# Performance work log

Measured on AMD Instinct MI355X. Metric: run time of the kernel, lower is better.

Reference implementation:

```python
import jax, jax.numpy as jnp
import numpy as np

N, P, IN_DIM, OUT_DIM = 8192, 16, 256, 128
HID = [512, 1024, 1024, 512]
MIN_VAR = 0.01


def setup_inputs() -> dict:
    key = jax.random.key(0)
    ks = jax.random.split(key, 12)
    s = 0.05
    inp = {
        "x": jax.random.normal(ks[0], (N, P, IN_DIM), dtype=jnp.float32),
        "mask": jnp.zeros((N, P), dtype=bool),
        # per-film input FiLM linears, stacked: [P, hid0, in_dim]
        "W_in": jax.random.normal(ks[1], (P, HID[0], IN_DIM), dtype=jnp.float32) * s,
        "b_in": jax.random.normal(ks[2], (P, HID[0]), dtype=jnp.float32) * s,
        # shared trunk layers hidden_dims[i] -> hidden_dims[i+1]
        "W1": jax.random.normal(ks[3], (HID[1], HID[0]), dtype=jnp.float32) * s,
        "b1": jax.random.normal(ks[4], (HID[1],), dtype=jnp.float32) * s,
        "W2": jax.random.normal(ks[5], (HID[2], HID[1]), dtype=jnp.float32) * s,
        "b2": jax.random.normal(ks[6], (HID[2],), dtype=jnp.float32) * s,
        "W3": jax.random.normal(ks[7], (HID[3], HID[2]), dtype=jnp.float32) * s,
        "b3": jax.random.normal(ks[8], (HID[3],), dtype=jnp.float32) * s,
        # per-film output FiLM linears: [P, 2*out_dim, hid_last]
        "W_out": jax.random.normal(ks[9], (P, 2 * OUT_DIM, HID[3]), dtype=jnp.float32) * s,
        "b_out": jax.random.normal(ks[10], (P, 2 * OUT_DIM), dtype=jnp.float32) * s,
    }
    return inp


def reference(x, mask, W_in, b_in, W1, b1, W2, b2, W3, b3, W_out, b_out):
    # per-film input linear (no activation after it, matching original)
    h = jnp.einsum("npd,phd->nph", x, W_in) + b_in            # [N,P,hid0]
    # shared trunk: activation after each layer
    h = jax.nn.relu(jnp.einsum("nph,oh->npo", h, W1) + b1)    # [N,P,hid1]
    h = jax.nn.relu(jnp.einsum("nph,oh->npo", h, W2) + b2)    # [N,P,hid2]
    h = jax.nn.relu(jnp.einsum("nph,oh->npo", h, W3) + b3)    # [N,P,hid3]
    # per-film output linear (no activation)
    out = jnp.einsum("nph,poh->npo", h, W_out) + b_out        # [N,P,2*out_dim]
    mu = out[..., :OUT_DIM]
    var = MIN_VAR + (1.0 - MIN_VAR) * jax.nn.softplus(out[..., OUT_DIM:])
    # masked (mask==True) positions stay NaN, matching the torch scatter into nan-filled tensors
    nan = jnp.float32(jnp.nan)
    m = mask[..., None]
    mu = jnp.where(m, nan, mu)
    var = jnp.where(m, nan, var)
    return mu, var
```

## Files before the change

### kernel.cpp

```cpp
#include <hip/hip_runtime.h>
#include <stdint.h>

typedef __attribute__((ext_vector_type(8))) short short8;
typedef __attribute__((ext_vector_type(4))) float f32x4;
typedef __attribute__((ext_vector_type(4))) unsigned short u16x4;

#define NTOK 8192
#define PDIM 16
#define ODIM 128

__device__ __forceinline__ uint16_t f2bf(float f) {
    uint32_t u = __builtin_bit_cast(uint32_t, f);
    u += 0x7FFFu + ((u >> 16) & 1u);
    return (uint16_t)(u >> 16);
}

__global__ void convert_f32_bf16(const float* __restrict__ in, uint16_t* __restrict__ out, int n4) {
    int i = blockIdx.x * blockDim.x + threadIdx.x;
    if (i >= n4) return;
    f32x4 v = ((const f32x4*)in)[i];
    u16x4 o;
    o[0] = f2bf(v[0]); o[1] = f2bf(v[1]); o[2] = f2bf(v[2]); o[3] = f2bf(v[3]);
    ((u16x4*)out)[i] = o;
}

template<int EPI>
__global__ __launch_bounds__(512, 1)
void gemm3(const uint16_t* __restrict__ A, int lda, long long Abatch,
           const uint16_t* __restrict__ B, int ldb, long long Bbatch,
           const float* __restrict__ bias, int biasBatch,
           uint16_t* __restrict__ C, int ldc, long long Cbatch,
           int K, int gridN, int gridM,
           const unsigned char* __restrict__ mask,
           float* __restrict__ outv)
{
    __shared__ uint16_t lds[73728];

    const int tid  = threadIdx.x;
    const int wid  = tid >> 6;
    const int lane = tid & 63;
    const int l15  = lane & 15;
    const int kg   = lane >> 4;
    const int wm   = wid >> 2;
    const int wn   = wid & 3;

    const int nwg = (int)gridDim.x;
    int id = (int)blockIdx.x;
    id = (id & 7) * (nwg >> 3) + (id >> 3);
    const int n_blk = id % gridN;
    const int rest  = id / gridN;
    const int m_blk = rest % gridM;
    const int p     = rest / gridM;

    const int m0 = m_blk * 128;
    const int n0 = n_blk * 256;

    const uint16_t* Ap = A + (long long)p * Abatch;
    const uint16_t* Bp = B + (long long)p * Bbatch;

    const int c3 = tid >> 3;
    const int k8 = ((tid & 7) ^ (c3 & 7)) * 8;
    const uint16_t* sA0 = Ap + (long long)(m0 + c3) * lda + k8;
    const uint16_t* sA1 = sA0 + (long long)64 * lda;
    const uint16_t* sB0 = Bp + (long long)(n0 + c3) * ldb + k8;
    const uint16_t* sB1 = sB0 + (long long)64 * ldb;
    const uint16_t* sB2 = sB0 + (long long)128 * ldb;
    const uint16_t* sB3 = sB0 + (long long)192 * ldb;
    const int dW = wid * 512;

#define GLL(SRC, DST) __builtin_amdgcn_global_load_lds( \
        (const __attribute__((address_space(1))) void*)(SRC), \
        (__attribute__((address_space(3))) void*)(&lds[DST]), 16, 0, 0)

    auto stage = [&](int kt, int bb) {
        const int o = kt * 64;
        GLL(sA0 + o, bb + dW);
        GLL(sA1 + o, bb + 4096 + dW);
        GLL(sB0 + o, bb + 8192 + dW);
        GLL(sB1 + o, bb + 12288 + dW);
        GLL(sB2 + o, bb + 16384 + dW);
        GLL(sB3 + o, bb + 20480 + dW);
    };

    const int cs0 = (kg ^ (l15 & 7)) * 8;
    const int cs1 = ((kg + 4) ^ (l15 & 7)) * 8;
    const int rX = (wm * 64 + l15) * 64;
    const int rW = 8192 + (wn * 64 + l15) * 64;

    f32x4 acc[4][4];
    #pragma unroll
    for (int i = 0; i < 4; ++i)
        #pragma unroll
        for (int j = 0; j < 4; ++j)
            acc[i][j] = (f32x4){0.f, 0.f, 0.f, 0.f};

    const int NT = K >> 6;
    stage(0, 0);
    stage(1, 24576);
    asm volatile("s_waitcnt vmcnt(6)\ns_barrier" ::: "memory");

    int cur = 0;
    for (int t = 0; t < NT; ++t) {
        const int bb = cur * 24576;
        short8 xf[4][2], wfa[2][2], wfb[2][2];
        #pragma unroll
        for (int mi = 0; mi < 4; ++mi) {
            xf[mi][0] = *(const short8*)&lds[bb + rX + mi * 1024 + cs0];
            xf[mi][1] = *(const short8*)&lds[bb + rX + mi * 1024 + cs1];
        }
        #pragma unroll
        for (int ni = 0; ni < 2; ++ni) {
            wfa[ni][0] = *(const short8*)&lds[bb + rW + ni * 1024 + cs0];
            wfa[ni][1] = *(const short8*)&lds[bb + rW + ni * 1024 + cs1];
        }
        const bool more = (t + 2 < NT);
        if (more) stage(t + 2, (cur == 0 ? 2 : cur - 1) * 24576);
        #pragma unroll
        for (int ni = 0; ni < 2; ++ni)
            #pragma unroll
            for (int mi = 0; mi < 4; ++mi) {
                acc[ni][mi] = __builtin_amdgcn_mfma_f32_16x16x32_bf16(wfa[ni][0], xf[mi][0], acc[ni][mi], 0, 0, 0);
                acc[ni][mi] = __builtin_amdgcn_mfma_f32_16x16x32_bf16(wfa[ni][1], xf[mi][1], acc[ni][mi], 0, 0, 0);
            }
        #pragma unroll
        for (int ni = 0; ni < 2; ++ni) {
            wfb[ni][0] = *(const short8*)&lds[bb + rW + (ni + 2) * 1024 + cs0];
            wfb[ni][1] = *(const short8*)&lds[bb + rW + (ni + 2) * 1024 + cs1];
        }
        #pragma unroll
        for (int ni = 0; ni < 2; ++ni)
            #pragma unroll
            for (int mi = 0; mi < 4; ++mi) {
                acc[ni + 2][mi] = __builtin_amdgcn_mfma_f32_16x16x32_bf16(wfb[ni][0], xf[mi][0], acc[ni + 2][mi], 0, 0, 0);
                acc[ni + 2][mi] = __builtin_amdgcn_mfma_f32_16x16x32_bf16(wfb[ni][1], xf[mi][1], acc[ni + 2][mi], 0, 0, 0);
            }
        if (more) asm volatile("s_waitcnt vmcnt(6) lgkmcnt(0)\ns_barrier" ::: "memory");
        else      asm volatile("s_waitcnt vmcnt(0) lgkmcnt(0)\ns_barrier" ::: "memory");
        cur = (cur == 2) ? 0 : cur + 1;
    }
#undef GLL

    if (EPI == 0 || EPI == 1) {
        uint16_t* Cp = C + (long long)p * Cbatch;
        const float* biasp = bias + (long long)p * biasBatch;
        #pragma unroll
        for (int ni = 0; ni < 4; ++ni) {
            const int gn = n0 + wn * 64 + ni * 16 + kg * 4;
            const f32x4 bv = *(const f32x4*)&biasp[gn];
            #pragma unroll
            for (int mi = 0; mi < 4; ++mi) {
                const int gm = m0 + wm * 64 + mi * 16 + l15;
                f32x4 v = acc[ni][mi];
                u16x4 o;
                #pragma unroll
                for (int j = 0; j < 4; ++j) {
                    float e = v[j] + bv[j];
                    if (EPI == 1) e = fmaxf(e, 0.f);
                    o[j] = f2bf(e);
                }
                *(u16x4*)&Cp[(long long)gm * ldc + gn] = o;
            }
        }
    } else {
        const long long VAROFF = (long long)NTOK * PDIM * ODIM;
        const float* biasp = bias + (long long)p * biasBatch;
        #pragma unroll
        for (int ni = 0; ni < 4; ++ni) {
            const int gn = n0 + wn * 64 + ni * 16 + kg * 4;
            const f32x4 bv = *(const f32x4*)&biasp[gn];
            #pragma unroll
            for (int mi = 0; mi < 4; ++mi) {
                const int gm = m0 + wm * 64 + mi * 16 + l15;
                const long long token = (long long)gm * PDIM + p;
                const bool msk = mask[token] != 0;
                f32x4 v = acc[ni][mi];
                f32x4 o;
                if (gn < ODIM) {
                    #pragma unroll
                    for (int j = 0; j < 4; ++j) {
                        float e = v[j] + bv[j];
                        o[j] = msk ? __builtin_nanf("") : e;
                    }
                    *(f32x4*)&outv[token * ODIM + gn] = o;
                } else {
                    #pragma unroll
                    for (int j = 0; j < 4; ++j) {
                        float e = v[j] + bv[j];
                        float sp = (e > 20.f) ? e : log1pf(expf(e));
                        float var = 0.01f + 0.99f * sp;
                        o[j] = msk ? __builtin_nanf("") : var;
                    }
                    *(f32x4*)&outv[VAROFF + token * ODIM + (gn - ODIM)] = o;
                }
            }
        }
    }
}

extern "C" void kernel_launch(void* const* d_in, const int* in_sizes, int n_in,
                              void* d_out, int out_size, void* d_ws, size_t ws_size,
                              hipStream_t stream)
{
    const float* x     = (const float*)d_in[0];
    const unsigned char* mask = (const unsigned char*)d_in[1];
    const float* W_in  = (const float*)d_in[2];
    const float* b_in  = (const float*)d_in[3];
    const float* W1    = (const float*)d_in[4];
    const float* b1    = (const float*)d_in[5];
    const float* W2    = (const float*)d_in[6];
    const float* b2    = (const float*)d_in[7];
    const float* W3    = (const float*)d_in[8];
    const float* b3    = (const float*)d_in[9];
    const float* W_out = (const float*)d_in[10];
    const float* b_out = (const float*)d_in[11];
    float* out = (float*)d_out;

    uint16_t* ws   = (uint16_t*)d_ws;
    uint16_t* Wib  = ws;
    uint16_t* W1b  = Wib + 2097152;
    uint16_t* W2b  = W1b + 524288;
    uint16_t* W3b  = W2b + 1048576;
    uint16_t* Wob  = W3b + 524288;
    uint16_t* base = Wob + 2097152;

    long long NC = 8192;
    while (NC > 128 && 12582912LL + NC * 73728LL > (long long)ws_size) NC >>= 1;

    uint16_t* xb   = base;
    uint16_t* bufA = xb   + NC * 4096;
    uint16_t* bufB = bufA + NC * 16384;

    auto conv = [&](const float* src, uint16_t* dst, long long n) {
        long long n4 = n >> 2;
        convert_f32_bf16<<<dim3((unsigned)((n4 + 255) / 256)), dim3(256), 0, stream>>>(src, dst, (int)n4);
    };
    conv(W_in,  Wib, 2097152);
    conv(W1,    W1b, 524288);
    conv(W2,    W2b, 1048576);
    conv(W3,    W3b, 524288);
    conv(W_out, Wob, 2097152);

    const int nChunks = (int)(NTOK / NC);
    for (int c = 0; c < nChunks; ++c) {
        const long long nb = (long long)c * NC;
        const int NB = (int)(NC / 128);
        conv(x + nb * PDIM * 256, xb, NC * PDIM * 256);
        gemm3<0><<<dim3((unsigned)(2 * NB * 16)), 512, 0, stream>>>(
            xb, 4096, 256, Wib, 256, 131072, b_in, 512,
            bufA, 8192, 512, 256, 2, NB, nullptr, nullptr);
        gemm3<1><<<dim3((unsigned)(4 * NB * 16)), 512, 0, stream>>>(
            bufA, 512, 0, W1b, 512, 0, b1, 0,
            bufB, 1024, 0, 512, 4, NB * 16, nullptr, nullptr);
        gemm3<1><<<dim3((unsigned)(4 * NB * 16)), 512, 0, stream>>>(
            bufB, 1024, 0, W2b, 1024, 0, b2, 0,
            bufA, 1024, 0, 1024, 4, NB * 16, nullptr, nullptr);
        gemm3<1><<<dim3((unsigned)(2 * NB * 16)), 512, 0, stream>>>(
            bufA, 1024, 0, W3b, 1024, 0, b3, 0,
            bufB, 512, 0, 1024, 2, NB * 16, nullptr, nullptr);
        gemm3<2><<<dim3((unsigned)(1 * NB * 16)), 512, 0, stream>>>(
            bufB, 8192, 512, Wob, 512, 131072, b_out, 256,
            nullptr, 0, 0, 512, 1, NB,
            mask + nb * PDIM, out + nb * PDIM * ODIM);
    }
}
```

Measured before the change: 1.290 ms.

## Merge conversion launches, prefetch earlier, add MFMA priority hints, split GEMM kernels

```diff
diff --git a/kernel.cpp b/kernel.cpp
--- a/kernel.cpp
+++ b/kernel.cpp
@@ -24,15 +24,39 @@
     ((u16x4*)out)[i] = o;
 }
 
+__global__ void convert_multi(
+    const float* __restrict__ s0, uint16_t* __restrict__ d0, long long e0,
+    const float* __restrict__ s1, uint16_t* __restrict__ d1, long long e1,
+    const float* __restrict__ s2, uint16_t* __restrict__ d2, long long e2,
+    const float* __restrict__ s3, uint16_t* __restrict__ d3, long long e3,
+    const float* __restrict__ s4, uint16_t* __restrict__ d4, long long e4,
+    const float* __restrict__ s5, uint16_t* __restrict__ d5, long long e5)
+{
+    long long i = (long long)blockIdx.x * blockDim.x + threadIdx.x;
+    if (i >= e5) return;
+    const float* s; uint16_t* d; long long b;
+    if      (i < e0) { s = s0; d = d0; b = 0;  }
+    else if (i < e1) { s = s1; d = d1; b = e0; }
+    else if (i < e2) { s = s2; d = d2; b = e1; }
+    else if (i < e3) { s = s3; d = d3; b = e2; }
+    else if (i < e4) { s = s4; d = d4; b = e3; }
+    else             { s = s5; d = d5; b = e4; }
+    const long long j = i - b;
+    f32x4 v = ((const f32x4*)s)[j];
+    u16x4 o;
+    o[0] = f2bf(v[0]); o[1] = f2bf(v[1]); o[2] = f2bf(v[2]); o[3] = f2bf(v[3]);
+    ((u16x4*)d)[j] = o;
+}
+
 template<int EPI>
-__global__ __launch_bounds__(512, 1)
-void gemm3(const uint16_t* __restrict__ A, int lda, long long Abatch,
-           const uint16_t* __restrict__ B, int ldb, long long Bbatch,
-           const float* __restrict__ bias, int biasBatch,
-           uint16_t* __restrict__ C, int ldc, long long Cbatch,
-           int K, int gridN, int gridM,
-           const unsigned char* __restrict__ mask,
-           float* __restrict__ outv)
+__device__ __forceinline__
+void gemm_body(const uint16_t* __restrict__ A, int lda, long long Abatch,
+               const uint16_t* __restrict__ B, int ldb, long long Bbatch,
+               const float* __restrict__ bias, int biasBatch,
+               uint16_t* __restrict__ C, int ldc, long long Cbatch,
+               int K, int gridN, int gridM,
+               const unsigned char* __restrict__ mask,
+               float* __restrict__ outv)
 {
     __shared__ uint16_t lds[73728];
 
@@ -102,6 +126,8 @@
     int cur = 0;
     for (int t = 0; t < NT; ++t) {
         const int bb = cur * 24576;
+        const bool more = (t + 2 < NT);
+        if (more) stage(t + 2, (cur == 0 ? 2 : cur - 1) * 24576);
         short8 xf[4][2], wfa[2][2], wfb[2][2];
         #pragma unroll
         for (int mi = 0; mi < 4; ++mi) {
@@ -113,8 +139,7 @@
             wfa[ni][0] = *(const short8*)&lds[bb + rW + ni * 1024 + cs0];
             wfa[ni][1] = *(const short8*)&lds[bb + rW + ni * 1024 + cs1];
         }
-        const bool more = (t + 2 < NT);
-        if (more) stage(t + 2, (cur == 0 ? 2 : cur - 1) * 24576);
+        __builtin_amdgcn_s_setprio(1);
         #pragma unroll
         for (int ni = 0; ni < 2; ++ni)
             #pragma unroll
@@ -122,11 +147,13 @@
                 acc[ni][mi] = __builtin_amdgcn_mfma_f32_16x16x32_bf16(wfa[ni][0], xf[mi][0], acc[ni][mi], 0, 0, 0);
                 acc[ni][mi] = __builtin_amdgcn_mfma_f32_16x16x32_bf16(wfa[ni][1], xf[mi][1], acc[ni][mi], 0, 0, 0);
             }
+        __builtin_amdgcn_s_setprio(0);
         #pragma unroll
         for (int ni = 0; ni < 2; ++ni) {
             wfb[ni][0] = *(const short8*)&lds[bb + rW + (ni + 2) * 1024 + cs0];
             wfb[ni][1] = *(const short8*)&lds[bb + rW + (ni + 2) * 1024 + cs1];
         }
+        __builtin_amdgcn_s_setprio(1);
         #pragma unroll
         for (int ni = 0; ni < 2; ++ni)
             #pragma unroll
@@ -134,6 +161,7 @@
                 acc[ni + 2][mi] = __builtin_amdgcn_mfma_f32_16x16x32_bf16(wfb[ni][0], xf[mi][0], acc[ni + 2][mi], 0, 0, 0);
                 acc[ni + 2][mi] = __builtin_amdgcn_mfma_f32_16x16x32_bf16(wfb[ni][1], xf[mi][1], acc[ni + 2][mi], 0, 0, 0);
             }
+        __builtin_amdgcn_s_setprio(0);
         if (more) asm volatile("s_waitcnt vmcnt(6) lgkmcnt(0)\ns_barrier" ::: "memory");
         else      asm volatile("s_waitcnt vmcnt(0) lgkmcnt(0)\ns_barrier" ::: "memory");
         cur = (cur == 2) ? 0 : cur + 1;
@@ -197,6 +225,21 @@
     }
 }
 
+#define GEMM_PARAMS const uint16_t* A, int lda, long long Abatch, \
+                    const uint16_t* B, int ldb, long long Bbatch, \
+                    const float* bias, int biasBatch, \
+                    uint16_t* C, int ldc, long long Cbatch, \
+                    int K, int gridN, int gridM, \
+                    const unsigned char* mask, float* outv
+#define GEMM_ARGS A, lda, Abatch, B, ldb, Bbatch, bias, biasBatch, C, ldc, Cbatch, \
+                  K, gridN, gridM, mask, outv
+
+__global__ __launch_bounds__(512, 1) void g_Lin (GEMM_PARAMS) { gemm_body<0>(GEMM_ARGS); }
+__global__ __launch_bounds__(512, 1) void g_L1  (GEMM_PARAMS) { gemm_body<1>(GEMM_ARGS); }
+__global__ __launch_bounds__(512, 1) void g_L2  (GEMM_PARAMS) { gemm_body<1>(GEMM_ARGS); }
+__global__ __launch_bounds__(512, 1) void g_L3  (GEMM_PARAMS) { gemm_body<1>(GEMM_ARGS); }
+__global__ __launch_bounds__(512, 1) void g_Lout(GEMM_PARAMS) { gemm_body<2>(GEMM_ARGS); }
+
 extern "C" void kernel_launch(void* const* d_in, const int* in_sizes, int n_in,
                               void* d_out, int out_size, void* d_ws, size_t ws_size,
                               hipStream_t stream)
@@ -230,34 +273,49 @@
     uint16_t* bufA = xb   + NC * 4096;
     uint16_t* bufB = bufA + NC * 16384;
 
-    auto conv = [&](const float* src, uint16_t* dst, long long n) {
-        long long n4 = n >> 2;
-        convert_f32_bf16<<<dim3((unsigned)((n4 + 255) / 256)), dim3(256), 0, stream>>>(src, dst, (int)n4);
-    };
-    conv(W_in,  Wib, 2097152);
-    conv(W1,    W1b, 524288);
-    conv(W2,    W2b, 1048576);
-    conv(W3,    W3b, 524288);
-    conv(W_out, Wob, 2097152);
+    if (NC == 8192) {
+        const long long e0 = 2097152 / 4;
+        const long long e1 = e0 + 524288 / 4;
+        const long long e2 = e1 + 1048576 / 4;
+        const long long e3 = e2 + 524288 / 4;
+        const long long e4 = e3 + 2097152 / 4;
+        const long long e5 = e4 + 33554432 / 4;
+        convert_multi<<<dim3((unsigned)((e5 + 255) / 256)), dim3(256), 0, stream>>>(
+            W_in, Wib, e0, W1, W1b, e1, W2, W2b, e2,
+            W3, W3b, e3, W_out, Wob, e4, x, xb, e5);
+    } else {
+        const long long e0 = 2097152 / 4;
+        const long long e1 = e0 + 524288 / 4;
+        const long long e2 = e1 + 1048576 / 4;
+        const long long e3 = e2 + 524288 / 4;
+        const long long e4 = e3 + 2097152 / 4;
+        convert_multi<<<dim3((unsigned)((e4 + 255) / 256)), dim3(256), 0, stream>>>(
+            W_in, Wib, e0, W1, W1b, e1, W2, W2b, e2,
+            W3, W3b, e3, W_out, Wob, e4, W_out, Wob, e4);
+    }
 
     const int nChunks = (int)(NTOK / NC);
     for (int c = 0; c < nChunks; ++c) {
         const long long nb = (long long)c * NC;
         const int NB = (int)(NC / 128);
-        conv(x + nb * PDIM * 256, xb, NC * PDIM * 256);
-        gemm3<0><<<dim3((unsigned)(2 * NB * 16)), 512, 0, stream>>>(
+        if (NC != 8192) {
+            long long n4 = (NC * PDIM * 256) >> 2;
+            convert_f32_bf16<<<dim3((unsigned)((n4 + 255) / 256)), dim3(256), 0, stream>>>(
+                x + nb * PDIM * 256, xb, (int)n4);
+        }
+        g_Lin<<<dim3((unsigned)(2 * NB * 16)), 512, 0, stream>>>(
             xb, 4096, 256, Wib, 256, 131072, b_in, 512,
             bufA, 8192, 512, 256, 2, NB, nullptr, nullptr);
-        gemm3<1><<<dim3((unsigned)(4 * NB * 16)), 512, 0, stream>>>(
+        g_L1<<<dim3((unsigned)(4 * NB * 16)), 512, 0, stream>>>(
             bufA, 512, 0, W1b, 512, 0, b1, 0,
             bufB, 1024, 0, 512, 4, NB * 16, nullptr, nullptr);
-        gemm3<1><<<dim3((unsigned)(4 * NB * 16)), 512, 0, stream>>>(
+        g_L2<<<dim3((unsigned)(4 * NB * 16)), 512, 0, stream>>>(
             bufB, 1024, 0, W2b, 1024, 0, b2, 0,
             bufA, 1024, 0, 1024, 4, NB * 16, nullptr, nullptr);
-        gemm3<1><<<dim3((unsigned)(2 * NB * 16)), 512, 0, stream>>>(
+        g_L3<<<dim3((unsigned)(2 * NB * 16)), 512, 0, stream>>>(
             bufA, 1024, 0, W3b, 1024, 0, b3, 0,
             bufB, 512, 0, 1024, 2, NB * 16, nullptr, nullptr);
-        gemm3<2><<<dim3((unsigned)(1 * NB * 16)), 512, 0, stream>>>(
+        g_Lout<<<dim3((unsigned)(1 * NB * 16)), 512, 0, stream>>>(
             bufB, 8192, 512, Wob, 512, 131072, b_out, 256,
             nullptr, 0, 0, 512, 1, NB,
             mask + nb * PDIM, out + nb * PDIM * ODIM);
```

Result: faster. 1.248 ms (-3.2%).
